# Performance work log

Measured on AMD Instinct MI355X. Metric: run time of the kernel, lower is better.

The kernel has to match this reference:

```python
import jax, jax.numpy as jnp
import numpy as np

MAX_SPAN_WIDTH = 30


def setup_inputs() -> dict:
    key = jax.random.key(0)
    ks = jax.random.split(key, 10)
    num_words, D = 1024, 768          # BERT-base hidden size
    num_spans = 8192                  # candidate spans
    feat, ffnn = 20, 1000             # feature_size, ffnn_size
    span_dim = 3 * D + feat           # 2324

    mention_doc = jax.random.normal(ks[0], (num_words, D), jnp.float32)
    starts = jax.random.randint(ks[1], (num_spans,), 0, num_words, jnp.int32)
    widths = jax.random.randint(ks[2], (num_spans,), 1, MAX_SPAN_WIDTH + 1, jnp.int32)
    ends = jnp.minimum(starts + widths - 1, num_words - 1).astype(jnp.int32)

    def lin(k, fan_in, shape):
        return (jax.random.normal(k, shape, jnp.float32) / np.sqrt(fan_in)).astype(jnp.float32)

    return {
        "mention_doc": mention_doc,
        "w_width_emb": jax.random.normal(ks[3], (MAX_SPAN_WIDTH, feat), jnp.float32) * 0.02,
        "w_head": lin(ks[4], D, (D,)),
        "b_head": jnp.zeros((), jnp.float32),
        "W1": lin(ks[5], span_dim, (span_dim, ffnn)),
        "b1": jnp.zeros((ffnn,), jnp.float32),
        "W2": lin(ks[6], ffnn, (ffnn, ffnn)),
        "b2": jnp.zeros((ffnn,), jnp.float32),
        "W3": lin(ks[7], ffnn, (ffnn, 1)),
        "b3": jnp.zeros((1,), jnp.float32),
        "candidate_starts": starts,
        "candidate_ends": ends,
        "top_span_num": 409,  # min(3900, int(1024 * 0.4))
    }


def _span_scores(mention_doc, w_width_emb, w_head, b_head, W1, b1, W2, b2, W3, b3,
                 starts, ends):
    num_words = mention_doc.shape[0]
    start_emb = mention_doc[starts]                       # [S, D]
    end_emb = mention_doc[ends]                           # [S, D]
    span_widths = ends - starts + 1
    width_emb = w_width_emb[span_widths - 1]              # [S, F]
    # span word indices, clamped (same as torch.clamp(..., max=num_words-1))
    idxes = jnp.minimum(jnp.arange(MAX_SPAN_WIDTH, dtype=starts.dtype)[None, :]
                        + starts[:, None], num_words - 1)  # [S, W]
    head_scores = mention_doc @ w_head + b_head            # [num_words]
    hs = head_scores[idxes]                                # [S, W]
    mask = jnp.arange(MAX_SPAN_WIDTH)[None, :] < span_widths[:, None]
    hs = jnp.where(mask, hs, -jnp.inf)
    attn = jax.nn.softmax(hs, axis=1)                      # [S, W]
    attended = jnp.einsum("sw,swd->sd", attn, mention_doc[idxes])  # [S, D]
    span_emb = jnp.concatenate([start_emb, end_emb, width_emb, attended], axis=-1)
    h = jax.nn.relu(span_emb @ W1 + b1)
    h = jax.nn.relu(h @ W2 + b2)
    return (h @ W3 + b3)[:, 0]                             # [S]


def _extract_top_spans(scores, starts, ends, top_span_num, num_words):
    """Greedy sorted selection with crossing-span (NMS-style) suppression."""
    order = jnp.argsort(-scores)                           # descending by score
    pos = jnp.arange(num_words)

    def step(carry, span_idx):
        max_end, min_start, count, selected = carry
        s = starts[span_idx]
        e = ends[span_idx]
        dup = e == max_end[s]                              # same (start, max-end) already chosen
        cross1 = jnp.any((pos > s) & (pos <= e) & (max_end > e))
        cross2 = jnp.any((pos >= s) & (pos < e) & (min_start < s))
        accept = (count < top_span_num) & ~dup & ~cross1 & ~cross2
        max_end = max_end.at[s].max(jnp.where(accept, e, -1))
        min_start = min_start.at[e].min(jnp.where(accept, s, num_words))
        w = jnp.minimum(count, top_span_num - 1)
        selected = selected.at[w].set(
            jnp.where(accept, span_idx.astype(jnp.int32), selected[w]))
        return (max_end, min_start, count + accept.astype(jnp.int32), selected), None

    init = (jnp.full((num_words,), -1, jnp.int32),
            jnp.full((num_words,), num_words, jnp.int32),
            jnp.int32(0),
            jnp.full((top_span_num,), -1, jnp.int32))
    (_, _, _, selected), _ = jax.lax.scan(step, init, order.astype(jnp.int32))

    # final sort by (start, end); unfilled (-1) slots sort to the back
    big = num_words * num_words
    keys = jnp.where(selected >= 0,
                     starts[selected] * num_words + ends[selected], big)
    return selected[jnp.argsort(keys)]                     # [top_span_num], -1 padded


def reference(mention_doc, w_width_emb, w_head, b_head, W1, b1, W2, b2, W3, b3,
              candidate_starts, candidate_ends, top_span_num):
    scores = _span_scores(mention_doc, w_width_emb, w_head, b_head,
                          W1, b1, W2, b2, W3, b3,
                          candidate_starts, candidate_ends)
    top_idxes = _extract_top_spans(scores, candidate_starts, candidate_ends,
                                   int(top_span_num), mention_doc.shape[0])
    return scores, top_idxes
```

## Files before the change

### kernel.cpp

```cpp
#include <hip/hip_runtime.h>
#include <hip/hip_bf16.h>
#include <stdint.h>

#define NW   1024
#define D    768
#define NS   8192
#define MAXW 30
#define FFNN 1000
#define FEAT 20

typedef __attribute__((ext_vector_type(8))) short bf16x8;
typedef __attribute__((ext_vector_type(4))) float f32x4;
#define MFMA16 __builtin_amdgcn_mfma_f32_16x16x32_bf16

#define O_P    0
#define O_P4   3072000
#define O_HS   3102000
#define O_ATT  3103024
#define O_PS   3365168
#define O_H1R  3504432

__device__ inline ushort f2b(float v) {
    __hip_bfloat16 b = __float2bfloat16(v);
    return *(ushort*)&b;
}
__device__ inline float b2f(ushort u) {
    __hip_bfloat16 b = *(__hip_bfloat16*)&u;
    return __bfloat162float(b);
}

__global__ __launch_bounds__(256) void k_head(const float* __restrict__ doc,
                                              const float* __restrict__ wh,
                                              const float* __restrict__ bh,
                                              float* __restrict__ hs) {
    int wid = threadIdx.x >> 6, lane = threadIdx.x & 63;
    int word = blockIdx.x * 4 + wid;
    const float* row = doc + word * D;
    float acc = 0.f;
    for (int d = lane; d < D; d += 64) acc += row[d] * wh[d];
    #pragma unroll
    for (int o = 32; o; o >>= 1) acc += __shfl_down(acc, o);
    if (lane == 0) hs[word] = acc + bh[0];
}

__global__ __launch_bounds__(256) void k_p4(const float* __restrict__ wwe,
                                            const float* __restrict__ W1,
                                            float* __restrict__ P4) {
    int o = blockIdx.x * 256 + threadIdx.x;
    if (o >= 30 * FFNN) return;
    int wi = o / FFNN, j = o - wi * FFNN;
    float acc = 0.f;
    #pragma unroll
    for (int f = 0; f < FEAT; ++f) acc += wwe[wi * FEAT + f] * W1[(1536 + f) * FFNN + j];
    P4[o] = acc;
}

__global__ __launch_bounds__(256) void k_split(const float* __restrict__ src,
                                               ushort* __restrict__ h,
                                               ushort* __restrict__ l, int n) {
    int i = blockIdx.x * 256 + threadIdx.x;
    if (i >= n) return;
    float v = src[i];
    ushort hi = f2b(v);
    float r = v - b2f(hi);
    h[i] = hi;
    l[i] = f2b(r);
}

__global__ void k_tw1(const float* __restrict__ W1,
                      ushort* __restrict__ TH, ushort* __restrict__ TL) {
    __shared__ float tile[32][33];
    int tx = threadIdx.x, ty = threadIdx.y;
    int k0 = blockIdx.x * 32, n0 = blockIdx.y * 32, z = blockIdx.z;
    int roff = (z == 0) ? 0 : (z == 1) ? 768 : 1556;
    #pragma unroll
    for (int i = 0; i < 4; ++i) {
        int kk = ty + i * 8;
        float v = (n0 + tx < FFNN) ? W1[(size_t)(roff + k0 + kk) * FFNN + n0 + tx] : 0.f;
        tile[kk][tx] = v;
    }
    __syncthreads();
    #pragma unroll
    for (int i = 0; i < 4; ++i) {
        int nn = ty + i * 8;
        float v = tile[tx][nn];
        ushort hi = f2b(v);
        float r = v - b2f(hi);
        size_t o = (size_t)z * 1024 * D + (size_t)(n0 + nn) * D + k0 + tx;
        TH[o] = hi;
        TL[o] = f2b(r);
    }
}

__global__ void k_tw2(const float* __restrict__ W2,
                      ushort* __restrict__ TH, ushort* __restrict__ TL) {
    __shared__ float tile[32][33];
    int tx = threadIdx.x, ty = threadIdx.y;
    int k0 = blockIdx.x * 32, n0 = blockIdx.y * 32;
    #pragma unroll
    for (int i = 0; i < 4; ++i) {
        int kk = ty + i * 8;
        float v = (k0 + kk < FFNN && n0 + tx < FFNN)
                    ? W2[(size_t)(k0 + kk) * FFNN + n0 + tx] : 0.f;
        tile[kk][tx] = v;
    }
    __syncthreads();
    #pragma unroll
    for (int i = 0; i < 4; ++i) {
        int nn = ty + i * 8;
        int k = k0 + tx;
        float v = tile[tx][nn];
        ushort hi = f2b(v);
        float r = v - b2f(hi);
        size_t o = (size_t)(n0 + nn) * 1024 + k;
        TH[o] = hi;
        TL[o] = f2b(r);
    }
}

__global__ __launch_bounds__(256) void k_gemmPm(const ushort* __restrict__ Ah_g,
                                                const ushort* __restrict__ Al_g,
                                                const ushort* __restrict__ Bh_g,
                                                const ushort* __restrict__ Bl_g,
                                                float* __restrict__ Pout) {
    __shared__ ushort LDS[2][4][128 * 32];
    int tid = threadIdx.x;
    int orig = blockIdx.x;
    int t = (orig & 7) * 24 + (orig >> 3);
    int z = t >> 6, rem = t & 63;
    int rowt = rem & 7, colt = rem >> 3;
    int row0 = rowt * 128, col0 = colt * 128;
    size_t zoff = (size_t)z * 1024 * D;
    const ushort* Bh_z = Bh_g + zoff;
    const ushort* Bl_z = Bl_g + zoff;
    float* C = Pout + (size_t)z * NW * FFNN;
    int w = tid >> 6, l = tid & 63;
    int wr = w >> 1, wc = w & 1;
    int fr = l & 15, kb = l >> 4;
    int r0 = tid >> 2, p = tid & 3;
    int r1 = r0 + 64;
    int q0 = p ^ ((r0 >> 1) & 3);
    int q1 = p ^ ((r1 >> 1) & 3);
    int base0 = (w * 64) * 8;
    int base1 = (256 + w * 64) * 8;
    f32x4 acc[4][4] = {};
    int cur = 0;
    #define STAGE_P(d, kt)                                                                  \
        do {                                                                                \
            int kg0 = (kt) + q0 * 8, kg1 = (kt) + q1 * 8;                                   \
            __builtin_amdgcn_global_load_lds((const uint*)(Ah_g + (size_t)(row0 + r0) * D + kg0), (uint*)&LDS[d][0][base0], 16, 0, 0); \
            __builtin_amdgcn_global_load_lds((const uint*)(Al_g + (size_t)(row0 + r0) * D + kg0), (uint*)&LDS[d][1][base0], 16, 0, 0); \
            __builtin_amdgcn_global_load_lds((const uint*)(Bh_z + (size_t)(col0 + r0) * D + kg0), (uint*)&LDS[d][2][base0], 16, 0, 0); \
            __builtin_amdgcn_global_load_lds((const uint*)(Bl_z + (size_t)(col0 + r0) * D + kg0), (uint*)&LDS[d][3][base0], 16, 0, 0); \
            __builtin_amdgcn_global_load_lds((const uint*)(Ah_g + (size_t)(row0 + r1) * D + kg1), (uint*)&LDS[d][0][base1], 16, 0, 0); \
            __builtin_amdgcn_global_load_lds((const uint*)(Al_g + (size_t)(row0 + r1) * D + kg1), (uint*)&LDS[d][1][base1], 16, 0, 0); \
            __builtin_amdgcn_global_load_lds((const uint*)(Bh_z + (size_t)(col0 + r1) * D + kg1), (uint*)&LDS[d][2][base1], 16, 0, 0); \
            __builtin_amdgcn_global_load_lds((const uint*)(Bl_z + (size_t)(col0 + r1) * D + kg1), (uint*)&LDS[d][3][base1], 16, 0, 0); \
        } while (0)
    STAGE_P(0, 0);
    __syncthreads();
    for (int kt = 0; kt < D; kt += 32) {
        if (kt + 32 < D) STAGE_P(cur ^ 1, kt + 32);
        bf16x8 af[4], alf[4], bfr[4], blf[4];
        #pragma unroll
        for (int mt = 0; mt < 4; ++mt) {
            int r = wr * 64 + mt * 16 + fr;
            int sl = (kb ^ ((r >> 1) & 3)) * 8;
            af[mt]  = *(const bf16x8*)&LDS[cur][0][r * 32 + sl];
            alf[mt] = *(const bf16x8*)&LDS[cur][1][r * 32 + sl];
        }
        #pragma unroll
        for (int nt = 0; nt < 4; ++nt) {
            int c = wc * 64 + nt * 16 + fr;
            int sl = (kb ^ ((c >> 1) & 3)) * 8;
            bfr[nt] = *(const bf16x8*)&LDS[cur][2][c * 32 + sl];
            blf[nt] = *(const bf16x8*)&LDS[cur][3][c * 32 + sl];
        }
        #pragma unroll
        for (int mt = 0; mt < 4; ++mt)
            #pragma unroll
            for (int nt = 0; nt < 4; ++nt) {
                acc[mt][nt] = MFMA16(af[mt], bfr[nt], acc[mt][nt], 0, 0, 0);
                acc[mt][nt] = MFMA16(af[mt], blf[nt], acc[mt][nt], 0, 0, 0);
                acc[mt][nt] = MFMA16(alf[mt], bfr[nt], acc[mt][nt], 0, 0, 0);
            }
        __syncthreads();
        cur ^= 1;
    }
    #pragma unroll
    for (int mt = 0; mt < 4; ++mt)
        #pragma unroll
        for (int nt = 0; nt < 4; ++nt)
            #pragma unroll
            for (int r = 0; r < 4; ++r) {
                int row = row0 + wr * 64 + mt * 16 + kb * 4 + r;
                int col = col0 + wc * 64 + nt * 16 + fr;
                if (col < FFNN) C[(size_t)row * FFNN + col] = acc[mt][nt][r];
            }
}

__global__ __launch_bounds__(256) void k_gemm2m(const ushort* __restrict__ Ah_g,
                                                const ushort* __restrict__ Al_g,
                                                const ushort* __restrict__ Bh_g,
                                                const ushort* __restrict__ Bl_g,
                                                const float* __restrict__ b2,
                                                const float* __restrict__ W3,
                                                float* __restrict__ PS) {
    __shared__ ushort LDS[2][4][128 * 32];
    int tid = threadIdx.x;
    int orig = blockIdx.x;
    int xcd = orig & 7, idx = orig >> 3;
    int rowt = xcd * 8 + (idx & 7), colt = idx >> 3;
    int row0 = rowt * 128, col0 = colt * 128;
    int w = tid >> 6, l = tid & 63;
    int wr = w >> 1, wc = w & 1;
    int fr = l & 15, kb = l >> 4;
    int r0 = tid >> 2, p = tid & 3;
    int r1 = r0 + 64;
    int q0 = p ^ ((r0 >> 1) & 3);
    int q1 = p ^ ((r1 >> 1) & 3);
    int base0 = (w * 64) * 8;
    int base1 = (256 + w * 64) * 8;
    f32x4 acc[4][4] = {};
    int cur = 0;
    #define STAGE_2(d, kt)                                                                  \
        do {                                                                                \
            int kg0 = (kt) + q0 * 8, kg1 = (kt) + q1 * 8;                                   \
            __builtin_amdgcn_global_load_lds((const uint*)(Ah_g + (size_t)(row0 + r0) * 1000 + kg0), (uint*)&LDS[d][0][base0], 16, 0, 0); \
            __builtin_amdgcn_global_load_lds((const uint*)(Al_g + (size_t)(row0 + r0) * 1000 + kg0), (uint*)&LDS[d][1][base0], 16, 0, 0); \
            __builtin_amdgcn_global_load_lds((const uint*)(Bh_g + (size_t)(col0 + r0) * 1024 + kg0), (uint*)&LDS[d][2][base0], 16, 0, 0); \
            __builtin_amdgcn_global_load_lds((const uint*)(Bl_g + (size_t)(col0 + r0) * 1024 + kg0), (uint*)&LDS[d][3][base0], 16, 0, 0); \
            __builtin_amdgcn_global_load_lds((const uint*)(Ah_g + (size_t)(row0 + r1) * 1000 + kg1), (uint*)&LDS[d][0][base1], 16, 0, 0); \
            __builtin_amdgcn_global_load_lds((const uint*)(Al_g + (size_t)(row0 + r1) * 1000 + kg1), (uint*)&LDS[d][1][base1], 16, 0, 0); \
            __builtin_amdgcn_global_load_lds((const uint*)(Bh_g + (size_t)(col0 + r1) * 1024 + kg1), (uint*)&LDS[d][2][base1], 16, 0, 0); \
            __builtin_amdgcn_global_load_lds((const uint*)(Bl_g + (size_t)(col0 + r1) * 1024 + kg1), (uint*)&LDS[d][3][base1], 16, 0, 0); \
        } while (0)
    STAGE_2(0, 0);
    __syncthreads();
    for (int kt = 0; kt < 1024; kt += 32) {
        if (kt + 32 < 1024) STAGE_2(cur ^ 1, kt + 32);
        bf16x8 af[4], alf[4], bfr[4], blf[4];
        #pragma unroll
        for (int mt = 0; mt < 4; ++mt) {
            int r = wr * 64 + mt * 16 + fr;
            int sl = (kb ^ ((r >> 1) & 3)) * 8;
            af[mt]  = *(const bf16x8*)&LDS[cur][0][r * 32 + sl];
            alf[mt] = *(const bf16x8*)&LDS[cur][1][r * 32 + sl];
        }
        #pragma unroll
        for (int nt = 0; nt < 4; ++nt) {
            int c = wc * 64 + nt * 16 + fr;
            int sl = (kb ^ ((c >> 1) & 3)) * 8;
            bfr[nt] = *(const bf16x8*)&LDS[cur][2][c * 32 + sl];
            blf[nt] = *(const bf16x8*)&LDS[cur][3][c * 32 + sl];
        }
        #pragma unroll
        for (int mt = 0; mt < 4; ++mt)
            #pragma unroll
            for (int nt = 0; nt < 4; ++nt) {
                acc[mt][nt] = MFMA16(af[mt], bfr[nt], acc[mt][nt], 0, 0, 0);
                acc[mt][nt] = MFMA16(af[mt], blf[nt], acc[mt][nt], 0, 0, 0);
                acc[mt][nt] = MFMA16(alf[mt], bfr[nt], acc[mt][nt], 0, 0, 0);
            }
        __syncthreads();
        cur ^= 1;
    }
    float w3v[4], b2v[4];
    #pragma unroll
    for (int nt = 0; nt < 4; ++nt) {
        int col = col0 + wc * 64 + nt * 16 + fr;
        bool cv = col < FFNN;
        w3v[nt] = cv ? W3[col] : 0.f;
        b2v[nt] = cv ? b2[col] : 0.f;
    }
    #pragma unroll
    for (int mt = 0; mt < 4; ++mt) {
        #pragma unroll
        for (int r = 0; r < 4; ++r) {
            float pp = 0.f;
            #pragma unroll
            for (int nt = 0; nt < 4; ++nt) {
                float v = fmaxf(acc[mt][nt][r] + b2v[nt], 0.f);
                pp = fmaf(v, w3v[nt], pp);
            }
            pp += __shfl_xor(pp, 1);
            pp += __shfl_xor(pp, 2);
            pp += __shfl_xor(pp, 4);
            pp += __shfl_xor(pp, 8);
            if (fr == 0) {
                int row = row0 + wr * 64 + mt * 16 + kb * 4 + r;
                PS[row * 16 + colt * 2 + wc] = pp;
            }
        }
    }
}

__global__ __launch_bounds__(256) void k_attn(const float* __restrict__ hs,
                                              const int* __restrict__ starts,
                                              const int* __restrict__ ends,
                                              float* __restrict__ attn) {
    int s = blockIdx.x * 256 + threadIdx.x;
    if (s >= NS) return;
    int st = starts[s], en = ends[s];
    int width = en - st + 1;
    float v[MAXW];
    float mx = -3.0e38f;
    #pragma unroll
    for (int w = 0; w < MAXW; ++w) {
        int idx = st + w; if (idx > NW - 1) idx = NW - 1;
        float x = hs[idx];
        v[w] = (w < width) ? x : -3.0e38f;
        mx = fmaxf(mx, v[w]);
    }
    float sum = 0.f;
    #pragma unroll
    for (int w = 0; w < MAXW; ++w) { v[w] = expf(v[w] - mx); sum += v[w]; }
    float inv = 1.f / sum;
    #pragma unroll
    for (int w = 0; w < MAXW; ++w) attn[s * 32 + w] = v[w] * inv;
}

__global__ __launch_bounds__(256) void k_h1(const float* __restrict__ P,
                                            const float* __restrict__ P4,
                                            const float* __restrict__ attn,
                                            const float* __restrict__ b1,
                                            const int* __restrict__ starts,
                                            const int* __restrict__ ends,
                                            ushort* __restrict__ H1h,
                                            ushort* __restrict__ H1l) {
    int s = blockIdx.x;
    int tid = threadIdx.x;
    if (tid >= 250) return;
    int st = starts[s], en = ends[s];
    int width = en - st + 1;
    const float4* P1r = (const float4*)(P + (size_t)st * FFNN);
    const float4* P2r = (const float4*)(P + (size_t)NW * FFNN + (size_t)en * FFNN);
    const float*  P3  = P + 2 * (size_t)NW * FFNN;
    const float4* P4r = (const float4*)(P4 + (size_t)(width - 1) * FFNN);
    const float4* b1v = (const float4*)b1;
    const float*  ar  = attn + s * 32;
    float4 a = P1r[tid], b = P2r[tid], c = P4r[tid], d = b1v[tid];
    float4 acc = {a.x + b.x + c.x + d.x,
                  a.y + b.y + c.y + d.y,
                  a.z + b.z + c.z + d.z,
                  a.w + b.w + c.w + d.w};
    for (int w = 0; w < width; ++w) {
        float aw = ar[w];
        float4 p3 = ((const float4*)(P3 + (size_t)(st + w) * FFNN))[tid];
        acc.x = fmaf(aw, p3.x, acc.x);
        acc.y = fmaf(aw, p3.y, acc.y);
        acc.z = fmaf(aw, p3.z, acc.z);
        acc.w = fmaf(aw, p3.w, acc.w);
    }
    float rv[4] = {fmaxf(acc.x, 0.f), fmaxf(acc.y, 0.f), fmaxf(acc.z, 0.f), fmaxf(acc.w, 0.f)};
    ushort4 hi, lo;
    ushort* hp = (ushort*)&hi;
    ushort* lp = (ushort*)&lo;
    #pragma unroll
    for (int j = 0; j < 4; ++j) {
        ushort h = f2b(rv[j]);
        float r = rv[j] - b2f(h);
        hp[j] = h;
        lp[j] = f2b(r);
    }
    *(ushort4*)(H1h + (size_t)s * FFNN + tid * 4) = hi;
    *(ushort4*)(H1l + (size_t)s * FFNN + tid * 4) = lo;
}

__global__ __launch_bounds__(256) void k_score2(const float* __restrict__ PS,
                                                const float* __restrict__ b3,
                                                float* __restrict__ out) {
    int r = blockIdx.x * 256 + threadIdx.x;
    if (r >= NS) return;
    float s = 0.f;
    #pragma unroll
    for (int b = 0; b < 16; ++b) s += PS[r * 16 + b];
    out[r] = s + b3[0];
}

__global__ __launch_bounds__(256) void k_rankA(const float* __restrict__ scores,
                                               int* __restrict__ RANK) {
    __shared__ unsigned long long tile[256];
    int i = blockIdx.x * 256 + threadIdx.x;
    int j = blockIdx.y * 256 + threadIdx.x;
    unsigned uj = __float_as_uint(scores[j]);
    unsigned mj = (uj >> 31) ? ~uj : (uj | 0x80000000u);
    tile[threadIdx.x] = ((unsigned long long)(~mj) << 32) | (unsigned)j;
    __syncthreads();
    unsigned u = __float_as_uint(scores[i]);
    unsigned m = (u >> 31) ? ~u : (u | 0x80000000u);
    unsigned long long key = ((unsigned long long)(~m) << 32) | (unsigned)i;
    int r = 0;
    #pragma unroll 8
    for (int q = 0; q < 256; ++q) r += (tile[q] < key);
    if (r) atomicAdd(&RANK[i], r);
}

__global__ __launch_bounds__(256) void k_rankB(const int* __restrict__ RANK,
                                               const int* __restrict__ starts,
                                               const int* __restrict__ ends,
                                               unsigned long long* __restrict__ pk) {
    int i = blockIdx.x * 256 + threadIdx.x;
    pk[RANK[i]] = ((unsigned long long)(unsigned)i << 32) |
                  ((unsigned)starts[i] << 16) | (unsigned)ends[i];
}

__global__ __launch_bounds__(64) void k_masks(const unsigned long long* __restrict__ pk,
                                              unsigned long long* __restrict__ MC,
                                              unsigned long long* __restrict__ ME,
                                              unsigned long long* __restrict__ MG) {
    int lane = threadIdx.x;
    int c = blockIdx.x;
    unsigned long long p = pk[c * 64 + lane];
    int s = (int)((p >> 16) & 0xFFFF);
    int e = (int)(p & 0xFFFF);
    unsigned long long conf = 0, eqm = 0, gtm = 0;
    for (int r = 1; r < 64; ++r) {
        int j = (lane + r) & 63;
        int sj = __shfl(s, j);
        int ej = __shfl(e, j);
        unsigned long long bit = 1ull << j;
        bool cross = ((sj > s) & (sj <= e) & (ej > e)) |
                     ((ej >= s) & (ej < e) & (sj < s));
        if (cross) conf |= bit;
        if (sj == s) { if (ej == e) eqm |= bit; else if (ej > e) gtm |= bit; }
    }
    MC[c * 64 + lane] = conf;
    ME[c * 64 + lane] = eqm;
    MG[c * 64 + lane] = gtm;
}

__global__ __launch_bounds__(64) void k_scan(const unsigned long long* __restrict__ pk,
                                             const unsigned long long* __restrict__ MC,
                                             const unsigned long long* __restrict__ ME,
                                             const unsigned long long* __restrict__ MG,
                                             int top, int* __restrict__ SEL,
                                             int* __restrict__ SELKEY,
                                             int* __restrict__ CNT) {
    __shared__ int mxs[NW];
    __shared__ int mne[NW];
    __shared__ int mxe[NW];
    int lane = threadIdx.x;
    unsigned long long lower = (1ull << lane) - 1ull;
    for (int p = lane; p < NW; p += 64) { mxs[p] = -1; mne[p] = NW; mxe[p] = -1; }
    __syncthreads();
    int count = 0;
    unsigned long long pc = pk[lane];
    unsigned long long conf = MC[lane], eqm = ME[lane], gtm = MG[lane];
    for (int c = 0; c < NS / 64 && count < top; ++c) {
        unsigned long long pn = 0, cn = 0, en2 = 0, gn = 0;
        if (c + 1 < NS / 64) {
            int o = (c + 1) * 64 + lane;
            pn = pk[o]; cn = MC[o]; en2 = ME[o]; gn = MG[o];
        }
        int span = (int)(pc >> 32);
        int s = (int)((pc >> 16) & 0xFFFF);
        int e = (int)(pc & 0xFFFF);
        int bad = (mxs[e] > s) | (mne[s] < e);
        int g = mxe[s];
        bool gdup = (g == e), ggt = (g > e);
        unsigned long long pending = __ballot(!bad), committed = 0;
        unsigned long long relv = (conf | eqm | gtm) & lower;
        while (pending) {
            bool mine = (pending >> lane) & 1;
            bool ready = mine && ((pending & relv) == 0ull);
            unsigned long long cb = committed & lower;
            bool rej = (cb & conf) != 0ull;
            bool gt_any = ggt || ((cb & gtm) != 0ull);
            bool eq_any = gdup || ((cb & eqm) != 0ull);
            bool acc_now = ready && !rej && !(eq_any && !gt_any);
            committed |= __ballot(acc_now);
            pending &= ~__ballot(ready);
        }
        int allowed = top - count;
        while (__popcll(committed) > allowed)
            committed &= ~(1ull << (63 - __builtin_clzll(committed)));
        if ((committed >> lane) & 1) {
            int pos = count + __popcll(committed & lower);
            SEL[pos] = span;
            SELKEY[pos] = s * NW + e;
            atomicMax(&mxe[s], e);
            #pragma unroll
            for (int k = 0; k < MAXW - 1; ++k) {
                if (k < e - s) {
                    atomicMax(&mxs[s + k], s);
                    atomicMin(&mne[s + 1 + k], e);
                }
            }
        }
        count += __popcll(committed);
        __syncthreads();
        pc = pn; conf = cn; eqm = en2; gtm = gn;
    }
    if (lane == 0) *CNT = count;
}

__global__ __launch_bounds__(512) void k_sort(const int* __restrict__ SEL,
                                              const int* __restrict__ SELKEY,
                                              const int* __restrict__ CNT,
                                              int top, float* __restrict__ out_idx) {
    __shared__ int keys[512];
    __shared__ int vals[512];
    int cnt = *CNT;
    int r = threadIdx.x;
    if (r < top) {
        keys[r] = (r < cnt) ? SELKEY[r] : NW * NW;
        vals[r] = (r < cnt) ? SEL[r] : -1;
    }
    __syncthreads();
    if (r < top) {
        int kr = keys[r];
        int rank = 0;
        for (int q = 0; q < top; ++q) {
            int kq = keys[q];
            rank += (kq < kr) || (kq == kr && q < r);
        }
        out_idx[rank] = (float)vals[r];
    }
}

extern "C" void kernel_launch(void* const* d_in, const int* in_sizes, int n_in,
                              void* d_out, int out_size, void* d_ws, size_t ws_size,
                              hipStream_t stream) {
    const float* doc = (const float*)d_in[0];
    const float* wwe = (const float*)d_in[1];
    const float* wh  = (const float*)d_in[2];
    const float* bh  = (const float*)d_in[3];
    const float* W1  = (const float*)d_in[4];
    const float* b1  = (const float*)d_in[5];
    const float* W2  = (const float*)d_in[6];
    const float* b2  = (const float*)d_in[7];
    const float* W3  = (const float*)d_in[8];
    const float* b3  = (const float*)d_in[9];
    const int* starts = (const int*)d_in[10];
    const int* ends   = (const int*)d_in[11];
    int top = out_size - NS;

    float* ws  = (float*)d_ws;
    float* P   = ws + O_P;
    float* P4  = ws + O_P4;
    float* HS  = ws + O_HS;
    float* ATT = ws + O_ATT;
    float* PS  = ws + O_PS;
    float* H1R = ws + O_H1R;
    ushort* H1H = (ushort*)H1R;
    ushort* H1L = (ushort*)(H1R + 4096000);
    ushort* W1TH = (ushort*)H1R;
    ushort* W1TL = (ushort*)(H1R + 1179648);
    ushort* DOCH = (ushort*)(H1R + 2359296);
    ushort* DOCL = (ushort*)(H1R + 2752512);
    ushort* W2TH = (ushort*)ws;
    ushort* W2TL = (ushort*)(ws + 524288);
    unsigned long long* PK = (unsigned long long*)H1R;
    int* SEL    = (int*)(ws + O_ATT);
    int* SELKEY = SEL + 512;
    int* CNT    = SEL + 1024;
    int* RANK   = SEL + 2048;
    unsigned long long* MC = (unsigned long long*)(ws + O_PS);
    unsigned long long* ME = MC + NS;
    unsigned long long* MG = MC + 2 * NS;
    float* outs = (float*)d_out;

    k_head<<<NW / 4, 256, 0, stream>>>(doc, wh, bh, HS);
    k_p4<<<(30 * FFNN + 255) / 256, 256, 0, stream>>>(wwe, W1, P4);

    k_split<<<(NW * D + 255) / 256, 256, 0, stream>>>(doc, DOCH, DOCL, NW * D);
    {
        dim3 g(24, 32, 3), b(32, 8);
        k_tw1<<<g, b, 0, stream>>>(W1, W1TH, W1TL);
    }
    k_gemmPm<<<192, 256, 0, stream>>>(DOCH, DOCL, W1TH, W1TL, P);

    k_attn<<<NS / 256, 256, 0, stream>>>(HS, starts, ends, ATT);
    k_h1<<<NS, 256, 0, stream>>>(P, P4, ATT, b1, starts, ends, H1H, H1L);

    {
        dim3 g(32, 32), b(32, 8);
        k_tw2<<<g, b, 0, stream>>>(W2, W2TH, W2TL);
    }
    k_gemm2m<<<512, 256, 0, stream>>>(H1H, H1L, W2TH, W2TL, b2, W3, PS);

    k_score2<<<NS / 256, 256, 0, stream>>>(PS, b3, outs);

    hipMemsetAsync(RANK, 0, NS * sizeof(int), stream);
    {
        dim3 g(NS / 256, NS / 256);
        k_rankA<<<g, 256, 0, stream>>>(outs, RANK);
    }
    k_rankB<<<NS / 256, 256, 0, stream>>>(RANK, starts, ends, PK);
    k_masks<<<NS / 64, 64, 0, stream>>>(PK, MC, ME, MG);
    k_scan<<<1, 64, 0, stream>>>(PK, MC, ME, MG, top, SEL, SELKEY, CNT);
    k_sort<<<1, 512, 0, stream>>>(SEL, SELKEY, CNT, top, outs + NS);
}
```

Baseline: 232.6 us.

## Halve GEMM-P column tile to 64 and fuse span softmax into h1 kernel

The first-layer projection GEMM now uses 128x64 tiles, doubling the grid from 192 to 384 blocks so more compute units have work. Each wave computes a 64x32 sub-tile, and the LDS staging layout is flattened to match. Separately, the attention softmax kernel is removed: each h1 block loads its 30 head scores into shared memory and computes the softmax weights itself. This drops one kernel launch and the ATT global round-trip, at the cost of redundant exp work across threads and less operand reuse per GEMM tile.

```diff
diff --git a/kernel.cpp b/kernel.cpp
--- a/kernel.cpp
+++ b/kernel.cpp
@@ -123,13 +123,13 @@
                                                 const ushort* __restrict__ Bh_g,
                                                 const ushort* __restrict__ Bl_g,
                                                 float* __restrict__ Pout) {
-    __shared__ ushort LDS[2][4][128 * 32];
+    __shared__ ushort LDS[2][12288];
     int tid = threadIdx.x;
     int orig = blockIdx.x;
-    int t = (orig & 7) * 24 + (orig >> 3);
-    int z = t >> 6, rem = t & 63;
-    int rowt = rem & 7, colt = rem >> 3;
-    int row0 = rowt * 128, col0 = colt * 128;
+    int t = (orig & 7) * 48 + (orig >> 3);
+    int pair = t >> 4, colt = t & 15;
+    int z = pair >> 3, rowt = pair & 7;
+    int row0 = rowt * 128, col0 = colt * 64;
     size_t zoff = (size_t)z * 1024 * D;
     const ushort* Bh_z = Bh_g + zoff;
     const ushort* Bl_z = Bl_g + zoff;
@@ -137,49 +137,43 @@
     int w = tid >> 6, l = tid & 63;
     int wr = w >> 1, wc = w & 1;
     int fr = l & 15, kb = l >> 4;
-    int r0 = tid >> 2, p = tid & 3;
-    int r1 = r0 + 64;
-    int q0 = p ^ ((r0 >> 1) & 3);
-    int q1 = p ^ ((r1 >> 1) & 3);
-    int base0 = (w * 64) * 8;
-    int base1 = (256 + w * 64) * 8;
-    f32x4 acc[4][4] = {};
+    int rA = tid >> 2, p = tid & 3;
+    int q = p ^ ((rA >> 1) & 3);
+    f32x4 acc[4][2] = {};
     int cur = 0;
     #define STAGE_P(d, kt)                                                                  \
         do {                                                                                \
-            int kg0 = (kt) + q0 * 8, kg1 = (kt) + q1 * 8;                                   \
-            __builtin_amdgcn_global_load_lds((const uint*)(Ah_g + (size_t)(row0 + r0) * D + kg0), (uint*)&LDS[d][0][base0], 16, 0, 0); \
-            __builtin_amdgcn_global_load_lds((const uint*)(Al_g + (size_t)(row0 + r0) * D + kg0), (uint*)&LDS[d][1][base0], 16, 0, 0); \
-            __builtin_amdgcn_global_load_lds((const uint*)(Bh_z + (size_t)(col0 + r0) * D + kg0), (uint*)&LDS[d][2][base0], 16, 0, 0); \
-            __builtin_amdgcn_global_load_lds((const uint*)(Bl_z + (size_t)(col0 + r0) * D + kg0), (uint*)&LDS[d][3][base0], 16, 0, 0); \
-            __builtin_amdgcn_global_load_lds((const uint*)(Ah_g + (size_t)(row0 + r1) * D + kg1), (uint*)&LDS[d][0][base1], 16, 0, 0); \
-            __builtin_amdgcn_global_load_lds((const uint*)(Al_g + (size_t)(row0 + r1) * D + kg1), (uint*)&LDS[d][1][base1], 16, 0, 0); \
-            __builtin_amdgcn_global_load_lds((const uint*)(Bh_z + (size_t)(col0 + r1) * D + kg1), (uint*)&LDS[d][2][base1], 16, 0, 0); \
-            __builtin_amdgcn_global_load_lds((const uint*)(Bl_z + (size_t)(col0 + r1) * D + kg1), (uint*)&LDS[d][3][base1], 16, 0, 0); \
+            int kg = (kt) + q * 8;                                                          \
+            __builtin_amdgcn_global_load_lds((const uint*)(Ah_g + (size_t)(row0 + rA) * D + kg),      (uint*)&LDS[d][(0 * 256 + tid) * 8], 16, 0, 0); \
+            __builtin_amdgcn_global_load_lds((const uint*)(Ah_g + (size_t)(row0 + rA + 64) * D + kg), (uint*)&LDS[d][(1 * 256 + tid) * 8], 16, 0, 0); \
+            __builtin_amdgcn_global_load_lds((const uint*)(Al_g + (size_t)(row0 + rA) * D + kg),      (uint*)&LDS[d][(2 * 256 + tid) * 8], 16, 0, 0); \
+            __builtin_amdgcn_global_load_lds((const uint*)(Al_g + (size_t)(row0 + rA + 64) * D + kg), (uint*)&LDS[d][(3 * 256 + tid) * 8], 16, 0, 0); \
+            __builtin_amdgcn_global_load_lds((const uint*)(Bh_z + (size_t)(col0 + rA) * D + kg),      (uint*)&LDS[d][(4 * 256 + tid) * 8], 16, 0, 0); \
+            __builtin_amdgcn_global_load_lds((const uint*)(Bl_z + (size_t)(col0 + rA) * D + kg),      (uint*)&LDS[d][(5 * 256 + tid) * 8], 16, 0, 0); \
         } while (0)
     STAGE_P(0, 0);
     __syncthreads();
     for (int kt = 0; kt < D; kt += 32) {
         if (kt + 32 < D) STAGE_P(cur ^ 1, kt + 32);
-        bf16x8 af[4], alf[4], bfr[4], blf[4];
+        bf16x8 af[4], alf[4], bfr[2], blf[2];
         #pragma unroll
         for (int mt = 0; mt < 4; ++mt) {
             int r = wr * 64 + mt * 16 + fr;
             int sl = (kb ^ ((r >> 1) & 3)) * 8;
-            af[mt]  = *(const bf16x8*)&LDS[cur][0][r * 32 + sl];
-            alf[mt] = *(const bf16x8*)&LDS[cur][1][r * 32 + sl];
-        }
-        #pragma unroll
-        for (int nt = 0; nt < 4; ++nt) {
-            int c = wc * 64 + nt * 16 + fr;
+            af[mt]  = *(const bf16x8*)&LDS[cur][r * 32 + sl];
+            alf[mt] = *(const bf16x8*)&LDS[cur][4096 + r * 32 + sl];
+        }
+        #pragma unroll
+        for (int nt = 0; nt < 2; ++nt) {
+            int c = wc * 32 + nt * 16 + fr;
             int sl = (kb ^ ((c >> 1) & 3)) * 8;
-            bfr[nt] = *(const bf16x8*)&LDS[cur][2][c * 32 + sl];
-            blf[nt] = *(const bf16x8*)&LDS[cur][3][c * 32 + sl];
+            bfr[nt] = *(const bf16x8*)&LDS[cur][8192 + c * 32 + sl];
+            blf[nt] = *(const bf16x8*)&LDS[cur][10240 + c * 32 + sl];
         }
         #pragma unroll
         for (int mt = 0; mt < 4; ++mt)
             #pragma unroll
-            for (int nt = 0; nt < 4; ++nt) {
+            for (int nt = 0; nt < 2; ++nt) {
                 acc[mt][nt] = MFMA16(af[mt], bfr[nt], acc[mt][nt], 0, 0, 0);
                 acc[mt][nt] = MFMA16(af[mt], blf[nt], acc[mt][nt], 0, 0, 0);
                 acc[mt][nt] = MFMA16(alf[mt], bfr[nt], acc[mt][nt], 0, 0, 0);
@@ -190,11 +184,11 @@
     #pragma unroll
     for (int mt = 0; mt < 4; ++mt)
         #pragma unroll
-        for (int nt = 0; nt < 4; ++nt)
+        for (int nt = 0; nt < 2; ++nt)
             #pragma unroll
             for (int r = 0; r < 4; ++r) {
                 int row = row0 + wr * 64 + mt * 16 + kb * 4 + r;
-                int col = col0 + wc * 64 + nt * 16 + fr;
+                int col = col0 + wc * 32 + nt * 16 + fr;
                 if (col < FFNN) C[(size_t)row * FFNN + col] = acc[mt][nt][r];
             }
 }
@@ -295,57 +289,49 @@
     }
 }
 
-__global__ __launch_bounds__(256) void k_attn(const float* __restrict__ hs,
-                                              const int* __restrict__ starts,
-                                              const int* __restrict__ ends,
-                                              float* __restrict__ attn) {
-    int s = blockIdx.x * 256 + threadIdx.x;
-    if (s >= NS) return;
-    int st = starts[s], en = ends[s];
-    int width = en - st + 1;
-    float v[MAXW];
-    float mx = -3.0e38f;
-    #pragma unroll
-    for (int w = 0; w < MAXW; ++w) {
-        int idx = st + w; if (idx > NW - 1) idx = NW - 1;
-        float x = hs[idx];
-        v[w] = (w < width) ? x : -3.0e38f;
-        mx = fmaxf(mx, v[w]);
-    }
-    float sum = 0.f;
-    #pragma unroll
-    for (int w = 0; w < MAXW; ++w) { v[w] = expf(v[w] - mx); sum += v[w]; }
-    float inv = 1.f / sum;
-    #pragma unroll
-    for (int w = 0; w < MAXW; ++w) attn[s * 32 + w] = v[w] * inv;
-}
-
 __global__ __launch_bounds__(256) void k_h1(const float* __restrict__ P,
                                             const float* __restrict__ P4,
-                                            const float* __restrict__ attn,
+                                            const float* __restrict__ hs,
                                             const float* __restrict__ b1,
                                             const int* __restrict__ starts,
                                             const int* __restrict__ ends,
                                             ushort* __restrict__ H1h,
                                             ushort* __restrict__ H1l) {
+    __shared__ float shs[32];
     int s = blockIdx.x;
     int tid = threadIdx.x;
-    if (tid >= 250) return;
     int st = starts[s], en = ends[s];
     int width = en - st + 1;
+    if (tid < MAXW) {
+        int idx = st + tid; if (idx > NW - 1) idx = NW - 1;
+        shs[tid] = hs[idx];
+    }
+    __syncthreads();
+    float v[MAXW];
+    float mx = -3.0e38f;
+    #pragma unroll
+    for (int w = 0; w < MAXW; ++w) {
+        float x = shs[w];
+        v[w] = (w < width) ? x : -3.0e38f;
+        mx = fmaxf(mx, v[w]);
+    }
+    float sum = 0.f;
+    #pragma unroll
+    for (int w = 0; w < MAXW; ++w) { v[w] = expf(v[w] - mx); sum += v[w]; }
+    float inv = 1.f / sum;
+    if (tid >= 250) return;
     const float4* P1r = (const float4*)(P + (size_t)st * FFNN);
     const float4* P2r = (const float4*)(P + (size_t)NW * FFNN + (size_t)en * FFNN);
     const float*  P3  = P + 2 * (size_t)NW * FFNN;
     const float4* P4r = (const float4*)(P4 + (size_t)(width - 1) * FFNN);
     const float4* b1v = (const float4*)b1;
-    const float*  ar  = attn + s * 32;
     float4 a = P1r[tid], b = P2r[tid], c = P4r[tid], d = b1v[tid];
     float4 acc = {a.x + b.x + c.x + d.x,
                   a.y + b.y + c.y + d.y,
                   a.z + b.z + c.z + d.z,
                   a.w + b.w + c.w + d.w};
     for (int w = 0; w < width; ++w) {
-        float aw = ar[w];
+        float aw = v[w] * inv;
         float4 p3 = ((const float4*)(P3 + (size_t)(st + w) * FFNN))[tid];
         acc.x = fmaf(aw, p3.x, acc.x);
         acc.y = fmaf(aw, p3.y, acc.y);
@@ -540,7 +526,6 @@
     float* P   = ws + O_P;
     float* P4  = ws + O_P4;
     float* HS  = ws + O_HS;
-    float* ATT = ws + O_ATT;
     float* PS  = ws + O_PS;
     float* H1R = ws + O_H1R;
     ushort* H1H = (ushort*)H1R;
@@ -569,10 +554,9 @@
         dim3 g(24, 32, 3), b(32, 8);
         k_tw1<<<g, b, 0, stream>>>(W1, W1TH, W1TL);
     }
-    k_gemmPm<<<192, 256, 0, stream>>>(DOCH, DOCL, W1TH, W1TL, P);
-
-    k_attn<<<NS / 256, 256, 0, stream>>>(HS, starts, ends, ATT);
-    k_h1<<<NS, 256, 0, stream>>>(P, P4, ATT, b1, starts, ends, H1H, H1L);
+    k_gemmPm<<<384, 256, 0, stream>>>(DOCH, DOCL, W1TH, W1TL, P);
+
+    k_h1<<<NS, 256, 0, stream>>>(P, P4, HS, b1, starts, ends, H1H, H1L);
 
     {
         dim3 g(32, 32), b(32, 8);
```

New measurement: 231.3 us. No clear change (-0.5%).
